# Kernel tuning notes

Hardware: AMD Instinct MI355X
Metric: run time of the kernel (lower is better)

The kernel has to match this reference:

```python
import jax, jax.numpy as jnp
import numpy as np

B, N, D = 32, 2048, 768
DEPTH, HEADS, GRID, NC = 12, 12, 10, 40
T = GRID * GRID + 1          # 100 pillars + cls token
HD = D // HEADS
SCALE = HD ** -0.5
INTERVAL = 0.2
MLP_H = 4 * D
EPS = 1e-5


def setup_inputs() -> dict:
    key = jax.random.key(0)
    ks = list(jax.random.split(key, 12))
    n = lambda k, s, std: (jax.random.normal(k, s, dtype=jnp.float32) * std)
    return {
        "x": jax.random.uniform(ks[0], (B, N, 3), minval=-1.0, maxval=1.0, dtype=jnp.float32),
        "W1": n(ks[1], (6, 32), 0.1),
        "W2": n(ks[2], (32, 64), 0.1),
        "W3": n(ks[3], (64, 128), 0.1),
        "Wa": n(ks[4], (256, D), 0.05),
        "bn_g": jnp.ones((GRID * GRID,), jnp.float32),
        "bn_b": jnp.zeros((GRID * GRID,), jnp.float32),
        "bn_mean": jnp.zeros((GRID * GRID,), jnp.float32),
        "bn_var": jnp.ones((GRID * GRID,), jnp.float32),
        "cls_token": jnp.zeros((1, 1, D), jnp.float32),
        "pos_embed": n(ks[5], (1, T, D), 0.02),
        "ln1_g": jnp.ones((DEPTH, D), jnp.float32), "ln1_b": jnp.zeros((DEPTH, D), jnp.float32),
        "qkv_w": n(ks[6], (DEPTH, D, 3 * D), 0.01),
        "proj_w": n(ks[7], (DEPTH, D, D), 0.01), "proj_b": jnp.zeros((DEPTH, D), jnp.float32),
        "ln2_g": jnp.ones((DEPTH, D), jnp.float32), "ln2_b": jnp.zeros((DEPTH, D), jnp.float32),
        "fc1_w": n(ks[8], (DEPTH, D, MLP_H), 0.01), "fc1_b": jnp.zeros((DEPTH, MLP_H), jnp.float32),
        "fc2_w": n(ks[9], (DEPTH, MLP_H, D), 0.01), "fc2_b": jnp.zeros((DEPTH, D), jnp.float32),
        "norm_g": jnp.ones((D,), jnp.float32), "norm_b": jnp.zeros((D,), jnp.float32),
        "head_w": n(ks[10], (D, NC), 0.01), "head_b": jnp.zeros((NC,), jnp.float32),
    }


def _layer_norm(x, g, b):
    m = jnp.mean(x, -1, keepdims=True)
    v = jnp.mean(jnp.square(x - m), -1, keepdims=True)
    return (x - m) * jax.lax.rsqrt(v + EPS) * g + b


def reference(x, W1, W2, W3, Wa, bn_g, bn_b, bn_mean, bn_var, cls_token, pos_embed,
              ln1_g, ln1_b, qkv_w, proj_w, proj_b, ln2_g, ln2_b,
              fc1_w, fc1_b, fc2_w, fc2_b, norm_g, norm_b, head_w, head_b):
    # ---- Pillar encoder (voxel bucketing via segment ops) ----
    # torch code reorders columns (y,z,x)->(z,y,x); voxel index uses (y,x)
    p = x[..., jnp.array([1, 0, 2])]                     # [B,N,3] = (z,y,x)
    yx = jnp.clip(p[..., 1:] + 1.0, 0.0, 1.99)
    idx = jnp.floor(yx / INTERVAL).astype(jnp.int32)     # [B,N,2] in [0,GRID)
    cell = (idx[..., 0] * GRID + idx[..., 1]
            + jnp.arange(B, dtype=jnp.int32)[:, None] * GRID * GRID).reshape(-1)
    pf = p.reshape(-1, 3)                                # [B*N,3]
    S = B * GRID * GRID
    cnt = jax.ops.segment_sum(jnp.ones((B * N,), pf.dtype), cell, num_segments=S)
    centroid = jax.ops.segment_sum(pf, cell, num_segments=S) / jnp.maximum(cnt, 1.0)[:, None]
    aug = jnp.concatenate([pf, pf - centroid[cell]], -1)  # [B*N,6]
    h = jax.nn.relu(aug @ W1)
    h = jax.nn.relu(h @ W2)
    h = jax.nn.relu(h @ W3)                               # [B*N,128]
    pooled = jax.ops.segment_max(h, cell, num_segments=S)  # per-pillar max
    h2 = jax.nn.relu(jnp.concatenate([h, pooled[cell]], -1) @ Wa)  # [B*N,768]
    pillar = jax.ops.segment_max(h2, cell, num_segments=S)
    pillar = jnp.where(cnt[:, None] > 0, pillar, 0.0)     # empty cells stay zero
    seq = pillar.reshape(B, GRID * GRID, D)               # flatten order = y*GRID+x
    # BatchNorm1d(100) over the sequence-position channel (eval mode)
    inv = bn_g * jax.lax.rsqrt(bn_var + EPS)
    seq = (seq - bn_mean[None, :, None]) * inv[None, :, None] + bn_b[None, :, None]

    # ---- ViT stack ----
    tokens = jnp.concatenate([jnp.broadcast_to(cls_token, (B, 1, D)), seq], 1) + pos_embed

    def block(hh, prm):
        g1, b1, qw, pw, pb, g2, b2, f1w, f1b, f2w, f2b = prm
        y = _layer_norm(hh, g1, b1)
        qkv = (y @ qw).reshape(B, T, 3, HEADS, HD)
        q, k, v = qkv[:, :, 0], qkv[:, :, 1], qkv[:, :, 2]   # [B,T,H,hd]
        attn = jax.nn.softmax(jnp.einsum('bqhd,bkhd->bhqk', q, k) * SCALE, -1)
        o = jnp.einsum('bhqk,bkhd->bqhd', attn, v).reshape(B, T, D)
        hh = hh + o @ pw + pb
        y = _layer_norm(hh, g2, b2)
        y = jax.nn.gelu(y @ f1w + f1b, approximate=False)
        hh = hh + y @ f2w + f2b
        return hh, None

    prms = (ln1_g, ln1_b, qkv_w, proj_w, proj_b, ln2_g, ln2_b, fc1_w, fc1_b, fc2_w, fc2_b)
    tokens, _ = jax.lax.scan(block, tokens, prms)
    out = _layer_norm(tokens, norm_g, norm_b)[:, 0] @ head_w + head_b  # cls head
    return out
```

## Files before the change

### kernel.cpp

```cpp
#include <hip/hip_runtime.h>

typedef __bf16 bf8 __attribute__((ext_vector_type(8)));
typedef float  f4  __attribute__((ext_vector_type(4)));
typedef unsigned long long uptr;

__device__ __forceinline__ void gload16(const void* g, void* l){
  __builtin_amdgcn_global_load_lds(
      (const __attribute__((address_space(1))) unsigned int*)(uptr)g,
      (__attribute__((address_space(3))) unsigned int*)(uptr)l,
      16, 0, 0);
}


__global__ __launch_bounds__(256) void k_cell(const float* __restrict__ x, int* __restrict__ cellArr,
                                              float* __restrict__ cnt, float* __restrict__ cent){
  int p = blockIdx.x*256 + threadIdx.x;
  float x0 = x[p*3+0], x1 = x[p*3+1], x2 = x[p*3+2];
  float y0 = fminf(fmaxf(x0 + 1.0f, 0.0f), 1.99f);
  float y1 = fminf(fmaxf(x2 + 1.0f, 0.0f), 1.99f);
  int i0 = (int)floorf(y0 / 0.2f);
  int i1 = (int)floorf(y1 / 0.2f);
  int b = p >> 11;
  int cell = b*100 + i0*10 + i1;
  cellArr[p] = cell;
  atomicAdd(&cnt[cell], 1.0f);
  atomicAdd(&cent[cell*3+0], x1);
  atomicAdd(&cent[cell*3+1], x0);
  atomicAdd(&cent[cell*3+2], x2);
}

__global__ __launch_bounds__(256) void k_scan(const float* __restrict__ cnt,
                                              int* __restrict__ base, int* __restrict__ wptr){
  __shared__ int a[256];
  int tid = threadIdx.x;
  int start = tid*13, end = start+13; if (end > 3200) end = 3200;
  int local = 0;
  for (int i = start; i < end; i++) local += (int)cnt[i];
  a[tid] = local;
  __syncthreads();
  for (int off = 1; off < 256; off <<= 1){
    int t = (tid >= off) ? a[tid - off] : 0;
    __syncthreads();
    a[tid] += t;
    __syncthreads();
  }
  int run = a[tid] - local;
  for (int i = start; i < end; i++){
    base[i] = run; wptr[i] = run;
    run += (int)cnt[i];
  }
}

__global__ __launch_bounds__(256) void k_scatter(const int* __restrict__ cellArr,
                                                 int* __restrict__ wptr, int* __restrict__ order){
  int p = blockIdx.x*256 + threadIdx.x;
  int c = cellArr[p];
  int pos = atomicAdd(&wptr[c], 1);
  order[pos] = p;
}

__global__ __launch_bounds__(256) void k_pointmlp(const float* __restrict__ x,
    const float* __restrict__ W1, const float* __restrict__ W2, const float* __restrict__ W3,
    const float* __restrict__ cent, const float* __restrict__ cnt, const int* __restrict__ cellArr,
    const int* __restrict__ order, int* __restrict__ cellSlot, __bf16* __restrict__ A2){
  __shared__ float w1s[6*32];
  __shared__ float w2s[32*64];
  __shared__ float w3s[64*128];
  int tid = threadIdx.x;
  for (int i = tid; i < 192;  i += 256) w1s[i] = W1[i];
  for (int i = tid; i < 2048; i += 256) w2s[i] = W2[i];
  for (int i = tid; i < 8192; i += 256) w3s[i] = W3[i];
  __syncthreads();
  int s = blockIdx.x*256 + tid;
  int p = order[s];
  int cell = cellArr[p];
  cellSlot[s] = cell;
  float pf0 = x[p*3+1], pf1 = x[p*3+0], pf2 = x[p*3+2];
  float cc = fmaxf(cnt[cell], 1.0f);
  float a[6] = {pf0, pf1, pf2,
                pf0 - cent[cell*3+0]/cc, pf1 - cent[cell*3+1]/cc, pf2 - cent[cell*3+2]/cc};
  float h1[32];
  #pragma unroll
  for (int f = 0; f < 32; f++){
    float t = 0.f;
    #pragma unroll
    for (int i = 0; i < 6; i++) t += a[i]*w1s[i*32+f];
    h1[f] = fmaxf(t, 0.f);
  }
  float h2[64];
  #pragma unroll
  for (int f = 0; f < 64; f++){
    float t = 0.f;
    #pragma unroll
    for (int i = 0; i < 32; i++) t += h1[i]*w2s[i*64+f];
    h2[f] = fmaxf(t, 0.f);
  }
  for (int f0 = 0; f0 < 128; f0 += 8){
    __bf16 tmp[8];
    #pragma unroll
    for (int j = 0; j < 8; j++){
      float t = 0.f;
      #pragma unroll
      for (int i = 0; i < 64; i++) t += h2[i]*w3s[i*128+f0+j];
      tmp[j] = (__bf16)fmaxf(t, 0.f);
    }
    *reinterpret_cast<uint4*>(&A2[(size_t)s*256 + f0]) = *reinterpret_cast<uint4*>(tmp);
  }
}

__global__ __launch_bounds__(128) void k_poolh(const __bf16* __restrict__ A2,
    const int* __restrict__ base, const float* __restrict__ cnt, float* __restrict__ pooled){
  int c = blockIdx.x, f = threadIdx.x;
  int b0 = base[c], n = (int)cnt[c];
  float v = 0.f;
  for (int k = 0; k < n; k++) v = fmaxf(v, (float)A2[(size_t)(b0+k)*256 + f]);
  pooled[c*128 + f] = v;
}

__global__ __launch_bounds__(256) void k_fill(const float* __restrict__ pooled,
    const int* __restrict__ cellSlot, __bf16* __restrict__ A2){
  int idx = blockIdx.x*256 + threadIdx.x;
  int s = idx >> 4, f0 = (idx & 15) << 3;
  int cell = cellSlot[s];
  const float* pp = &pooled[cell*128 + f0];
  __bf16 tmp[8];
  #pragma unroll
  for (int j = 0; j < 8; j++) tmp[j] = (__bf16)pp[j];
  *reinterpret_cast<uint4*>(&A2[(size_t)s*256 + 128 + f0]) = *reinterpret_cast<uint4*>(tmp);
}

__global__ __launch_bounds__(256) void k_pillarpool(const __bf16* __restrict__ h2c,
    const int* __restrict__ base, const float* __restrict__ cnt, float* __restrict__ pillar){
  int c = blockIdx.x, tid = threadIdx.x;
  int b0 = base[c], n = (int)cnt[c];
  if (n == 0) return;
  for (int f = tid; f < 768; f += 256){
    float v = 0.f;
    for (int s = b0; s < b0 + n; s++) v = fmaxf(v, (float)h2c[(size_t)s*768 + f]);
    pillar[(size_t)c*768 + f] = v;
  }
}

__global__ void k_assemble(const float* __restrict__ pillar,
    const float* __restrict__ bn_g, const float* __restrict__ bn_b,
    const float* __restrict__ bn_mean, const float* __restrict__ bn_var,
    const float* __restrict__ cls_t, const float* __restrict__ pos,
    float* __restrict__ tokens){
  int idx = blockIdx.x*256 + threadIdx.x;
  int m = idx / 768, d = idx % 768;
  int b = m / 101, t = m % 101;
  float v;
  if (t == 0) v = cls_t[d];
  else {
    int s = t - 1;
    float pv = pillar[((size_t)b*100 + s)*768 + d];
    float inv = bn_g[s]*rsqrtf(bn_var[s] + 1e-5f);
    v = (pv - bn_mean[s])*inv + bn_b[s];
  }
  tokens[idx] = v + pos[t*768 + d];
}


__global__ __launch_bounds__(256) void k_transpose(const float* __restrict__ W, __bf16* __restrict__ Wt,
                                                   int K, int N){
  __shared__ float t[32][33];
  int n0 = blockIdx.x*32, k0 = blockIdx.y*32;
  int tx = threadIdx.x & 31, ty = threadIdx.x >> 5;
  #pragma unroll
  for (int i = 0; i < 32; i += 8){
    int k = k0 + ty + i, n = n0 + tx;
    t[ty+i][tx] = (k < K && n < N) ? W[(size_t)k*N + n] : 0.f;
  }
  __syncthreads();
  #pragma unroll
  for (int i = 0; i < 32; i += 8){
    int n = n0 + ty + i, k = k0 + tx;
    if (n < N && k < K) Wt[(size_t)n*K + k] = (__bf16)t[tx][ty+i];
  }
}

__global__ __launch_bounds__(256) void k_transpose_all(
    const float* __restrict__ qw, const float* __restrict__ pw,
    const float* __restrict__ f1, const float* __restrict__ f2,
    __bf16* __restrict__ wq, __bf16* __restrict__ wp,
    __bf16* __restrict__ w1, __bf16* __restrict__ w2){
  int id = blockIdx.x;
  size_t l = blockIdx.y;
  const float* W; __bf16* Wt; int K, N, kx, nx;
  if (id < 432){               W=qw+l*768*2304; Wt=wq+l*768*2304; K=768;  N=2304; kx=id%6;  nx=id/6; }
  else if (id < 576){ id-=432; W=pw+l*768*768;  Wt=wp+l*768*768;  K=768;  N=768;  kx=id%6;  nx=id/6; }
  else if (id < 1152){ id-=576;  W=f1+l*768*3072; Wt=w1+l*768*3072; K=768;  N=3072; kx=id%6;  nx=id/6; }
  else {               id-=1152; W=f2+l*3072*768; Wt=w2+l*3072*768; K=3072; N=768;  kx=id%24; nx=id/24; }
  __shared__ __bf16 t[32*136];
  int k0 = kx*128, n0 = nx*32;
  int tid = threadIdx.x;
  int kr = tid >> 3, nc = (tid & 7)*4;
  #pragma unroll
  for (int i = 0; i < 4; i++){
    int k = kr + i*32;
    float4 v = *reinterpret_cast<const float4*>(&W[(size_t)(k0+k)*N + n0 + nc]);
    float vv[4] = {v.x, v.y, v.z, v.w};
    #pragma unroll
    for (int jj = 0; jj < 4; jj++){
      int n = nc + jj;
      int slot = (k >> 3) ^ ((n >> 1) & 7);
      t[n*136 + slot*8 + (k & 7)] = (__bf16)vv[jj];
    }
  }
  __syncthreads();
  int nr = tid >> 4, sl = tid & 15;
  #pragma unroll
  for (int j = 0; j < 2; j++){
    int n = j*16 + nr;
    int slot = sl ^ ((n >> 1) & 7);
    *reinterpret_cast<uint4*>(&Wt[(size_t)(n0+n)*K + k0 + sl*8]) =
        *reinterpret_cast<uint4*>(&t[n*136 + slot*8]);
  }
}


__global__ __launch_bounds__(256) void k_gemm(const __bf16* __restrict__ A, const __bf16* __restrict__ Bt,
    const float* __restrict__ bias, const float* __restrict__ res,
    float* __restrict__ outF, __bf16* __restrict__ outB,
    int M, int N, int K, int act, int splitK){
  __shared__ alignas(16) __bf16 As[128*64];
  __shared__ alignas(16) __bf16 Bs[128*64];
  int tid  = threadIdx.x;
  int m0 = blockIdx.y*128, n0 = blockIdx.x*128;
  int z = blockIdx.z;
  int kLen = K / splitK, k0 = z*kLen;
  int wave = tid >> 6, lane = tid & 63;
  int wm = (wave >> 1)*64, wn = (wave & 1)*64;
  int r16 = lane & 15, q = lane >> 4;
  int srow = tid >> 3;
  int sslot = tid & 7;
  int slotX[2];
  #pragma unroll
  for (int kk = 0; kk < 2; kk++) slotX[kk] = ((kk*4 + q) ^ (r16 & 7)) * 8;
  f4 acc[4][4];
  #pragma unroll
  for (int i = 0; i < 4; i++)
    #pragma unroll
    for (int j = 0; j < 4; j++) acc[i][j] = (f4){0.f,0.f,0.f,0.f};

  for (int kt = k0; kt < k0 + kLen; kt += 64){
    #pragma unroll
    for (int rr = 0; rr < 4; rr++){
      int row = rr*32 + srow;
      int scol = kt + ((sslot ^ (row & 7)) * 8);
      int gm = m0 + row; if (gm >= M) gm = M - 1;
      gload16(A  + (size_t)gm*K + scol, (char*)As + rr*4096 + tid*16);
      int gn = n0 + row;
      gload16(Bt + (size_t)gn*K + scol, (char*)Bs + rr*4096 + tid*16);
    }
    __syncthreads();
    #pragma unroll
    for (int kk = 0; kk < 2; kk++){
      bf8 af[4], bq[4];
      #pragma unroll
      for (int i = 0; i < 4; i++) af[i] = *reinterpret_cast<const bf8*>(&As[(wm + i*16 + r16)*64 + slotX[kk]]);
      #pragma unroll
      for (int j = 0; j < 4; j++) bq[j] = *reinterpret_cast<const bf8*>(&Bs[(wn + j*16 + r16)*64 + slotX[kk]]);
      #pragma unroll
      for (int i = 0; i < 4; i++)
        #pragma unroll
        for (int j = 0; j < 4; j++)
          acc[i][j] = __builtin_amdgcn_mfma_f32_16x16x32_bf16(af[i], bq[j], acc[i][j], 0, 0, 0);
    }
    __syncthreads();
  }

  #pragma unroll
  for (int i = 0; i < 4; i++){
    #pragma unroll
    for (int j = 0; j < 4; j++){
      int nn = n0 + wn + j*16 + r16;
      float bv = (bias && z == 0) ? bias[nn] : 0.f;
      #pragma unroll
      for (int r = 0; r < 4; r++){
        int m = m0 + wm + i*16 + q*4 + r;
        if (m >= M) continue;
        float v = acc[i][j][r] + bv;
        if (splitK > 1){
          atomicAdd(&outF[(size_t)m*N + nn], v);
        } else {
          if (act == 1) v = fmaxf(v, 0.f);
          else if (act == 2) v = 0.5f*v*(1.f + erff(v*0.70710678118654752f));
          if (outB){
            outB[(size_t)m*N + nn] = (__bf16)v;
          } else {
            float rv = res ? res[(size_t)m*N + nn] : 0.f;
            outF[(size_t)m*N + nn] = rv + v;
          }
        }
      }
    }
  }
}


__global__ __launch_bounds__(256) void k_ln(const float* __restrict__ in, const float* __restrict__ g,
    const float* __restrict__ bta, __bf16* __restrict__ outB, float* __restrict__ outF, int rowMul){
  int orow = blockIdx.x;
  const float* xr = in + (size_t)orow*rowMul*768;
  int tid = threadIdx.x;
  float v0 = xr[tid], v1 = xr[tid+256], v2 = xr[tid+512];
  float s = v0+v1+v2, s2 = v0*v0 + v1*v1 + v2*v2;
  #pragma unroll
  for (int off = 32; off > 0; off >>= 1){ s += __shfl_xor(s, off); s2 += __shfl_xor(s2, off); }
  __shared__ float rs[4], rq[4];
  int w = tid >> 6;
  if ((tid & 63) == 0){ rs[w] = s; rq[w] = s2; }
  __syncthreads();
  s = rs[0]+rs[1]+rs[2]+rs[3]; s2 = rq[0]+rq[1]+rq[2]+rq[3];
  float mean = s*(1.f/768.f);
  float var  = s2*(1.f/768.f) - mean*mean;
  float rstd = rsqrtf(var + 1e-5f);
  size_t ob = (size_t)orow*768;
  float y0 = (v0-mean)*rstd*g[tid]     + bta[tid];
  float y1 = (v1-mean)*rstd*g[tid+256] + bta[tid+256];
  float y2 = (v2-mean)*rstd*g[tid+512] + bta[tid+512];
  if (outB){ outB[ob+tid]=(__bf16)y0; outB[ob+tid+256]=(__bf16)y1; outB[ob+tid+512]=(__bf16)y2; }
  else     { outF[ob+tid]=y0;         outF[ob+tid+256]=y1;         outF[ob+tid+512]=y2; }
}


#define PSS 136
#define VTS 136

__global__ __launch_bounds__(256, 3) void k_attn(const __bf16* __restrict__ qkvB, __bf16* __restrict__ o){
  __shared__ alignas(16) __bf16 smem[64*VTS + 64*PSS];
  __bf16* Vt = smem;
  __bf16* Ps = smem + 64*VTS;
  int bh = blockIdx.x >> 1, half = blockIdx.x & 1;
  int b = bh / 12, h = bh % 12;
  int tid = threadIdx.x;
  const __bf16* basep = qkvB + (size_t)(b*101)*2304 + h*64;

  #pragma unroll
  for (int it = 0; it < 4; it++){
    int c = tid + it*256;
    int t = c >> 3, d0 = c & 7;
    bf8 v;
    if (t < 101){
      v = *reinterpret_cast<const bf8*>(&basep[(size_t)t*2304 + 1536 + d0*8]);
    } else {
      #pragma unroll
      for (int j = 0; j < 8; j++) v[j] = (__bf16)0.f;
    }
    #pragma unroll
    for (int j = 0; j < 8; j++){
      int jj = (j + d0) & 7;
      Vt[(d0*8 + jj)*VTS + t] = v[jj];
    }
  }

  int wave = tid >> 6, lane = tid & 63;
  int r16 = lane & 15, q = lane >> 4;
  int m0 = half*64 + wave*16;

  f4 sacc[7];
  #pragma unroll
  for (int j = 0; j < 7; j++) sacc[j] = (f4){0.f,0.f,0.f,0.f};
  #pragma unroll
  for (int kt = 0; kt < 64; kt += 32){
    int row = m0 + r16; if (row > 100) row = 100;
    bf8 aq = *reinterpret_cast<const bf8*>(&basep[(size_t)row*2304 + kt + q*8]);
    #pragma unroll
    for (int j = 0; j < 7; j++){
      int krow = j*16 + r16; if (krow > 100) krow = 100;
      bf8 kf = *reinterpret_cast<const bf8*>(&basep[(size_t)krow*2304 + 768 + kt + q*8]);
      sacc[j] = __builtin_amdgcn_mfma_f32_16x16x32_bf16(aq, kf, sacc[j], 0, 0, 0);
    }
  }

  #pragma unroll
  for (int r = 0; r < 4; r++){
    float s[7];
    #pragma unroll
    for (int j = 0; j < 7; j++){
      s[j] = sacc[j][r] * 0.125f;
      if (j == 6 && r16 >= 5) s[j] = -1e30f;
    }
    float mx = s[0];
    #pragma unroll
    for (int j = 1; j < 7; j++) mx = fmaxf(mx, s[j]);
    #pragma unroll
    for (int off2 = 1; off2 < 16; off2 <<= 1) mx = fmaxf(mx, __shfl_xor(mx, off2));
    float p[7], sum = 0.f;
    #pragma unroll
    for (int j = 0; j < 7; j++){ p[j] = __expf(s[j] - mx); sum += p[j]; }
    #pragma unroll
    for (int off2 = 1; off2 < 16; off2 <<= 1) sum += __shfl_xor(sum, off2);
    float inv = 1.f / sum;
    int lr = wave*16 + q*4 + r;
    #pragma unroll
    for (int j = 0; j < 7; j++) Ps[lr*PSS + j*16 + r16] = (__bf16)(p[j]*inv);
    Ps[lr*PSS + 112 + r16] = (__bf16)0.f;
  }
  __syncthreads();

  f4 oacc[4];
  #pragma unroll
  for (int n = 0; n < 4; n++) oacc[n] = (f4){0.f,0.f,0.f,0.f};
  #pragma unroll
  for (int kt = 0; kt < 128; kt += 32){
    bf8 af = *reinterpret_cast<const bf8*>(&Ps[(wave*16 + r16)*PSS + kt + q*8]);
    #pragma unroll
    for (int n = 0; n < 4; n++){
      bf8 bq = *reinterpret_cast<const bf8*>(&Vt[(n*16 + r16)*VTS + kt + q*8]);
      oacc[n] = __builtin_amdgcn_mfma_f32_16x16x32_bf16(af, bq, oacc[n], 0, 0, 0);
    }
  }

  #pragma unroll
  for (int n = 0; n < 4; n++){
    #pragma unroll
    for (int r = 0; r < 4; r++){
      int t = m0 + q*4 + r;
      if (t < 101)
        o[((size_t)(b*101 + t))*768 + h*64 + n*16 + r16] = (__bf16)oacc[n][r];
    }
  }
}

__global__ __launch_bounds__(256) void k_head(const float* __restrict__ cls, const float* __restrict__ hw,
                       const float* __restrict__ hb, float* __restrict__ out){
  int b = blockIdx.x;
  int tid = threadIdx.x;
  int c = tid % 40, s = tid / 40;
  __shared__ float part[6][40];
  if (s < 6){
    float acc = 0.f;
    for (int k = s*128; k < s*128 + 128; k++) acc += cls[b*768 + k]*hw[k*40 + c];
    part[s][c] = acc;
  }
  __syncthreads();
  if (tid < 40){
    float v = hb[tid];
    #pragma unroll
    for (int i = 0; i < 6; i++) v += part[i][tid];
    out[b*40 + tid] = v;
  }
}


extern "C" void kernel_launch(void* const* d_in, const int* in_sizes, int n_in,
                              void* d_out, int out_size, void* d_ws, size_t ws_size,
                              hipStream_t stream){
  const float* x       = (const float*)d_in[0];
  const float* W1      = (const float*)d_in[1];
  const float* W2      = (const float*)d_in[2];
  const float* W3      = (const float*)d_in[3];
  const float* Wa      = (const float*)d_in[4];
  const float* bn_g    = (const float*)d_in[5];
  const float* bn_b    = (const float*)d_in[6];
  const float* bn_mean = (const float*)d_in[7];
  const float* bn_var  = (const float*)d_in[8];
  const float* cls_t   = (const float*)d_in[9];
  const float* pos     = (const float*)d_in[10];
  const float* ln1_g   = (const float*)d_in[11];
  const float* ln1_b   = (const float*)d_in[12];
  const float* qkv_w   = (const float*)d_in[13];
  const float* proj_w  = (const float*)d_in[14];
  const float* proj_b  = (const float*)d_in[15];
  const float* ln2_g   = (const float*)d_in[16];
  const float* ln2_b   = (const float*)d_in[17];
  const float* fc1_w   = (const float*)d_in[18];
  const float* fc1_b   = (const float*)d_in[19];
  const float* fc2_w   = (const float*)d_in[20];
  const float* fc2_b   = (const float*)d_in[21];
  const float* norm_g  = (const float*)d_in[22];
  const float* norm_b  = (const float*)d_in[23];
  const float* head_w  = (const float*)d_in[24];
  const float* head_b  = (const float*)d_in[25];

  char* ws = (char*)d_ws;
  size_t off = 0;
  auto alloc = [&](size_t bytes)->void*{ void* p = ws + off; off += (bytes + 255) & ~(size_t)255; return p; };
  float* cnt     = (float*)alloc(3200*4);
  float* cent    = (float*)alloc(3200*3*4);
  float* pillar  = (float*)alloc((size_t)3200*768*4);
  size_t zbytes  = (size_t)((char*)pillar - (char*)cnt) + (size_t)3200*768*4;
  int*   base    = (int*)  alloc(3200*4);
  int*   wptr    = (int*)  alloc(3200*4);
  int*   order   = (int*)  alloc((size_t)65536*4);
  int*   cellSlot= (int*)  alloc((size_t)65536*4);
  int*   cellArr = (int*)  alloc((size_t)65536*4);
  float* pooled  = (float*)alloc((size_t)3200*128*4);
  float* tokens  = (float*)alloc((size_t)3232*768*4);
  float* cls     = (float*)alloc((size_t)32*768*4);
  __bf16* wWa    = (__bf16*)alloc((size_t)768*256*2);
  __bf16* wq12   = (__bf16*)alloc((size_t)12*768*2304*2);
  __bf16* wp12   = (__bf16*)alloc((size_t)12*768*768*2);
  __bf16* w112   = (__bf16*)alloc((size_t)12*768*3072*2);
  __bf16* w212   = (__bf16*)alloc((size_t)12*3072*768*2);
  size_t offR = off;
  __bf16* A2  = (__bf16*)alloc((size_t)65536*256*2);
  __bf16* h2c = (__bf16*)alloc((size_t)65536*768*2);
  size_t endPillarPhase = off;
  off = offR;
  __bf16* y    = (__bf16*)alloc((size_t)3232*768*2);
  __bf16* qkvB = (__bf16*)alloc((size_t)3232*2304*2);
  __bf16* o    = (__bf16*)alloc((size_t)3232*768*2);
  __bf16* mlp  = (__bf16*)alloc((size_t)3232*3072*2);
  if (off < endPillarPhase) off = endPillarPhase;
  (void)ws_size; (void)in_sizes; (void)n_in; (void)out_size;

  hipMemsetAsync(cnt, 0, zbytes, stream);

  k_transpose_all<<<dim3(1728,12),256,0,stream>>>(qkv_w, proj_w, fc1_w, fc2_w, wq12, wp12, w112, w212);
  k_transpose<<<dim3(24,8),256,0,stream>>>(Wa, wWa, 256, 768);

  k_cell<<<256,256,0,stream>>>(x, cellArr, cnt, cent);
  k_scan<<<1,256,0,stream>>>(cnt, base, wptr);
  k_scatter<<<256,256,0,stream>>>(cellArr, wptr, order);
  k_pointmlp<<<256,256,0,stream>>>(x, W1, W2, W3, cent, cnt, cellArr, order, cellSlot, A2);
  k_poolh<<<3200,128,0,stream>>>(A2, base, cnt, pooled);
  k_fill<<<4096,256,0,stream>>>(pooled, cellSlot, A2);
  k_gemm<<<dim3(6,512),256,0,stream>>>(A2, wWa, nullptr, nullptr, nullptr, h2c, 65536, 768, 256, 1, 1);
  k_pillarpool<<<3200,256,0,stream>>>(h2c, base, cnt, pillar);
  k_assemble<<<9696,256,0,stream>>>(pillar, bn_g, bn_b, bn_mean, bn_var, cls_t, pos, tokens);

  for (int l = 0; l < 12; l++){
    __bf16* wq = wq12 + (size_t)l*768*2304;
    __bf16* wp = wp12 + (size_t)l*768*768;
    __bf16* w1 = w112 + (size_t)l*768*3072;
    __bf16* w2 = w212 + (size_t)l*3072*768;
    k_ln<<<3232,256,0,stream>>>(tokens, ln1_g + l*768, ln1_b + l*768, y, nullptr, 1);
    k_gemm<<<dim3(18,26),256,0,stream>>>(y, wq, nullptr, nullptr, nullptr, qkvB, 3232, 2304, 768, 0, 1);
    k_attn<<<768,256,0,stream>>>(qkvB, o);
    k_gemm<<<dim3(6,26,4),256,0,stream>>>(o, wp, proj_b + l*768, nullptr, tokens, nullptr,
                                          3232, 768, 768, 0, 4);
    k_ln<<<3232,256,0,stream>>>(tokens, ln2_g + l*768, ln2_b + l*768, y, nullptr, 1);
    k_gemm<<<dim3(24,26),256,0,stream>>>(y, w1, fc1_b + l*3072, nullptr, nullptr, mlp, 3232, 3072, 768, 2, 1);
    k_gemm<<<dim3(6,26,4),256,0,stream>>>(mlp, w2, fc2_b + l*768, nullptr, tokens, nullptr,
                                          3232, 768, 3072, 0, 4);
  }

  k_ln<<<32,256,0,stream>>>(tokens, norm_g, norm_b, nullptr, cls, 101);
  k_head<<<32,256,0,stream>>>(cls, head_w, head_b, (float*)d_out);
}
```

Before: 2.826 ms.

## Remap GEMM and attention workgroups per XCD and fold Wa transpose into batch kernel

```diff
diff --git a/kernel.cpp b/kernel.cpp
--- a/kernel.cpp
+++ b/kernel.cpp
@@ -9,6 +9,12 @@
       (const __attribute__((address_space(1))) unsigned int*)(uptr)g,
       (__attribute__((address_space(3))) unsigned int*)(uptr)l,
       16, 0, 0);
+}
+
+__device__ __forceinline__ int xcd_chunk(int d, int nwg){
+  int q = nwg >> 3, r = nwg & 7;
+  int c = d & 7, j = d >> 3;
+  return c*q + (c < r ? c : r) + j;
 }
 
 
@@ -160,34 +166,21 @@
   tokens[idx] = v + pos[t*768 + d];
 }
 
-
-__global__ __launch_bounds__(256) void k_transpose(const float* __restrict__ W, __bf16* __restrict__ Wt,
-                                                   int K, int N){
-  __shared__ float t[32][33];
-  int n0 = blockIdx.x*32, k0 = blockIdx.y*32;
-  int tx = threadIdx.x & 31, ty = threadIdx.x >> 5;
-  #pragma unroll
-  for (int i = 0; i < 32; i += 8){
-    int k = k0 + ty + i, n = n0 + tx;
-    t[ty+i][tx] = (k < K && n < N) ? W[(size_t)k*N + n] : 0.f;
-  }
-  __syncthreads();
-  #pragma unroll
-  for (int i = 0; i < 32; i += 8){
-    int n = n0 + ty + i, k = k0 + tx;
-    if (n < N && k < K) Wt[(size_t)n*K + k] = (__bf16)t[tx][ty+i];
-  }
-}
-
 __global__ __launch_bounds__(256) void k_transpose_all(
     const float* __restrict__ qw, const float* __restrict__ pw,
     const float* __restrict__ f1, const float* __restrict__ f2,
+    const float* __restrict__ wa,
     __bf16* __restrict__ wq, __bf16* __restrict__ wp,
-    __bf16* __restrict__ w1, __bf16* __restrict__ w2){
+    __bf16* __restrict__ w1, __bf16* __restrict__ w2,
+    __bf16* __restrict__ wwa){
   int id = blockIdx.x;
   size_t l = blockIdx.y;
   const float* W; __bf16* Wt; int K, N, kx, nx;
-  if (id < 432){               W=qw+l*768*2304; Wt=wq+l*768*2304; K=768;  N=2304; kx=id%6;  nx=id/6; }
+  if (id >= 1728){
+    if (l != 0) return;
+    id -= 1728; W=wa; Wt=wwa; K=256; N=768; kx=id%2; nx=id/2;
+  }
+  else if (id < 432){          W=qw+l*768*2304; Wt=wq+l*768*2304; K=768;  N=2304; kx=id%6;  nx=id/6; }
   else if (id < 576){ id-=432; W=pw+l*768*768;  Wt=wp+l*768*768;  K=768;  N=768;  kx=id%6;  nx=id/6; }
   else if (id < 1152){ id-=576;  W=f1+l*768*3072; Wt=w1+l*768*3072; K=768;  N=3072; kx=id%6;  nx=id/6; }
   else {               id-=1152; W=f2+l*3072*768; Wt=w2+l*3072*768; K=3072; N=768;  kx=id%24; nx=id/24; }
@@ -226,7 +219,11 @@
   __shared__ alignas(16) __bf16 As[128*64];
   __shared__ alignas(16) __bf16 Bs[128*64];
   int tid  = threadIdx.x;
-  int m0 = blockIdx.y*128, n0 = blockIdx.x*128;
+  int gx = gridDim.x, gy = gridDim.y;
+  int d = blockIdx.y*gx + blockIdx.x;
+  int w = xcd_chunk(d, gx*gy);
+  int nx = w / gy, my = w % gy;
+  int m0 = my*128, n0 = nx*128;
   int z = blockIdx.z;
   int kLen = K / splitK, k0 = z*kLen;
   int wave = tid >> 6, lane = tid & 63;
@@ -332,7 +329,8 @@
   __shared__ alignas(16) __bf16 smem[64*VTS + 64*PSS];
   __bf16* Vt = smem;
   __bf16* Ps = smem + 64*VTS;
-  int bh = blockIdx.x >> 1, half = blockIdx.x & 1;
+  int w = xcd_chunk(blockIdx.x, gridDim.x);
+  int bh = w >> 1, half = w & 1;
   int b = bh / 12, h = bh % 12;
   int tid = threadIdx.x;
   const __bf16* basep = qkvB + (size_t)(b*101)*2304 + h*64;
@@ -509,8 +507,8 @@
 
   hipMemsetAsync(cnt, 0, zbytes, stream);
 
-  k_transpose_all<<<dim3(1728,12),256,0,stream>>>(qkv_w, proj_w, fc1_w, fc2_w, wq12, wp12, w112, w212);
-  k_transpose<<<dim3(24,8),256,0,stream>>>(Wa, wWa, 256, 768);
+  k_transpose_all<<<dim3(1776,12),256,0,stream>>>(qkv_w, proj_w, fc1_w, fc2_w, Wa,
+                                                  wq12, wp12, w112, w212, wWa);
 
   k_cell<<<256,256,0,stream>>>(x, cellArr, cnt, cent);
   k_scan<<<1,256,0,stream>>>(cnt, base, wptr);
```

Result: no change. 2.830 ms (+0.2%).
